# Optimization experiments

Hardware: AMD Instinct MI355X
Metric: run time of the kernel (lower is better)

The kernel has to match this reference:

```python
import jax, jax.numpy as jnp
import numpy as np

N_NODES = 50000
N_EDGES = 800000


def graph_conv(h, W, b, src, dst, n_nodes):
    # DGL GraphConv with norm='both':
    #   out = D_in^{-1/2} * A^T * (D_out^{-1/2} * h) @ W + b
    ones = jnp.ones((src.shape[0],), dtype=h.dtype)
    deg_out = jax.ops.segment_sum(ones, src, num_segments=n_nodes)
    deg_in = jax.ops.segment_sum(ones, dst, num_segments=n_nodes)
    norm_src = jnp.clip(deg_out, 1.0) ** -0.5  # [N]
    norm_dst = jnp.clip(deg_in, 1.0) ** -0.5   # [N]
    msg = (h * norm_src[:, None])[src]          # [E, F] gather
    agg = jax.ops.segment_sum(msg, dst, num_segments=n_nodes)  # [N, F] scatter
    return (agg * norm_dst[:, None]) @ W + b


def setup_inputs() -> dict:
    key = jax.random.key(0)
    ks = jax.random.split(key, 5)
    h = jax.random.normal(ks[0], (N_NODES, 64), dtype=jnp.float32)
    src = jax.random.randint(ks[1], (N_EDGES,), 0, N_NODES, dtype=jnp.int32)
    dst = jax.random.randint(ks[2], (N_EDGES,), 0, N_NODES, dtype=jnp.int32)
    W1 = jax.random.normal(ks[3], (64, 128), dtype=jnp.float32) * (1.0 / np.sqrt(64))
    b1 = jnp.zeros((128,), dtype=jnp.float32)
    W2 = jax.random.normal(ks[4], (128, 64), dtype=jnp.float32) * (1.0 / np.sqrt(128))
    b2 = jnp.zeros((64,), dtype=jnp.float32)
    return {"h": h, "src": src, "dst": dst, "W1": W1, "b1": b1, "W2": W2, "b2": b2}


def reference(h, src, dst, W1, b1, W2, b2):
    n = h.shape[0]
    h1 = jax.nn.relu(graph_conv(h, W1, b1, src, dst, n))
    out = graph_conv(h1, W2, b2, src, dst, n)
    return out
```

## Files before the change

### kernel.cpp

```cpp
#include <hip/hip_runtime.h>


#define NBMAX 512
#define CAPLOG 12
#define CAP (1 << CAPLOG)

typedef __attribute__((ext_vector_type(8))) short bf16x8;
typedef __attribute__((ext_vector_type(4))) float f32x4;

__device__ inline unsigned short f2bf(float f) {
    unsigned int u = __float_as_uint(f);
    unsigned int r = (u + 0x7FFFu + ((u >> 16) & 1u)) >> 16;
    return (unsigned short)r;
}
__device__ inline float bf2f_lo(unsigned int u) { return __uint_as_float(u << 16); }
__device__ inline float bf2f_hi(unsigned int u) { return __uint_as_float(u & 0xFFFF0000u); }
__device__ inline float bf2f(unsigned short h) {
    return __uint_as_float((unsigned int)h << 16);
}

__global__ __launch_bounds__(256) void place_direct(const int* __restrict__ src,
        const int* __restrict__ dst, int* __restrict__ cnt_s, int* __restrict__ cnt_d,
        unsigned char* __restrict__ ss, unsigned int* __restrict__ sd,
        int n_edges, int nb) {
    __shared__ int hs[NBMAX], hd[NBMAX], bs[NBMAX], bd[NBMAX];
    for (int i = threadIdx.x; i < nb; i += 256) { hs[i] = 0; hd[i] = 0; }
    __syncthreads();
    int chunk = (n_edges + gridDim.x - 1) / gridDim.x;
    int e0 = blockIdx.x * chunk;
    int e1 = e0 + chunk; if (e1 > n_edges) e1 = n_edges;
    for (int e = e0 + (int)threadIdx.x; e < e1; e += 256) {
        atomicAdd(&hs[src[e] >> 7], 1);
        atomicAdd(&hd[dst[e] >> 7], 1);
    }
    __syncthreads();
    for (int i = threadIdx.x; i < nb; i += 256) {
        int v = hs[i]; bs[i] = v ? atomicAdd(&cnt_s[i], v) : 0; hs[i] = 0;
        v = hd[i];     bd[i] = v ? atomicAdd(&cnt_d[i], v) : 0; hd[i] = 0;
    }
    __syncthreads();
    for (int e = e0 + (int)threadIdx.x; e < e1; e += 256) {
        int s = src[e], d = dst[e];
        int sb = s >> 7, db = d >> 7;
        int ps = bs[sb] + atomicAdd(&hs[sb], 1);
        ss[((size_t)sb << CAPLOG) + ps] = (unsigned char)(s & 127);
        int pd = bd[db] + atomicAdd(&hd[db], 1);
        sd[((size_t)db << CAPLOG) + pd] = ((unsigned int)(d & 127) << 25) | (unsigned int)s;
    }
}

__global__ __launch_bounds__(256) void prep(const float* __restrict__ h,
        const unsigned char* __restrict__ ss, const int* __restrict__ cnt_s,
        const unsigned int* __restrict__ sd, const int* __restrict__ cnt_d,
        float* __restrict__ norm_src, unsigned short* __restrict__ xb,
        int2* __restrict__ node_rng, unsigned short* __restrict__ srt,
        float* __restrict__ norm_dst, int n) {
    __shared__ int cnt[128], cur[128];
    __shared__ float nrm[128];
    __shared__ int w0tot;
    const int b = blockIdx.x;
    const int tid = threadIdx.x;

    if (tid < 128) cnt[tid] = 0;
    __syncthreads();
    {
        int used = cnt_s[b];
        const unsigned char* p = ss + ((size_t)b << CAPLOG);
        for (int i = tid; i < used; i += 256) atomicAdd(&cnt[p[i]], 1);
    }
    __syncthreads();
    if (tid < 128) {
        int c = cnt[tid]; if (c < 1) c = 1;
        float s = 1.0f / sqrtf((float)c);
        nrm[tid] = s;
        int node = (b << 7) + tid;
        if (node < n) norm_src[node] = s;
    }
    __syncthreads();
    {
        int base = b << 7;
        for (int t = tid; t < 128 * 16; t += 256) {
            int r = t >> 4, c4 = (t & 15) << 2;
            int node = base + r;
            if (node < n) {
                float s = nrm[r];
                float4 v = *(const float4*)(h + (size_t)node * 64 + c4);
                ushort4 o;
                o.x = f2bf(v.x * s); o.y = f2bf(v.y * s);
                o.z = f2bf(v.z * s); o.w = f2bf(v.w * s);
                *(ushort4*)(xb + (size_t)node * 64 + c4) = o;
            }
        }
    }
    __syncthreads();

    if (tid < 128) cnt[tid] = 0;
    __syncthreads();
    int used = cnt_d[b];
    const unsigned int* p = sd + ((size_t)b << CAPLOG);
    for (int i = tid; i < used; i += 256) atomicAdd(&cnt[p[i] >> 25], 1);
    __syncthreads();
    int lane = tid & 63, wid = tid >> 6;
    int v = (tid < 128) ? cnt[tid] : 0;
    int incl = v;
    #pragma unroll
    for (int d = 1; d < 64; d <<= 1) {
        int t = __shfl_up(incl, d, 64);
        if (lane >= d) incl += t;
    }
    if (tid == 63) w0tot = incl;
    __syncthreads();
    if (tid < 128) {
        int excl = incl - v + (wid == 1 ? w0tot : 0);
        cur[tid] = excl;
        int node = (b << 7) + tid;
        if (node < n) {
            int base = b << CAPLOG;
            node_rng[node] = make_int2(base + excl, base + excl + v);
            int c = v; if (c < 1) c = 1;
            norm_dst[node] = 1.0f / sqrtf((float)c);
        }
    }
    __syncthreads();
    for (int i = tid; i < used; i += 256) {
        unsigned int e = p[i];
        int l = (int)(e >> 25);
        int pos = atomicAdd(&cur[l], 1);
        srt[((size_t)b << CAPLOG) + pos] = (unsigned short)(e & 0xFFFFu);
    }
}

__global__ __launch_bounds__(256) void gather24(const unsigned short* __restrict__ xb,
        const unsigned short* __restrict__ srt, const int2* __restrict__ node_rng,
        const float* __restrict__ nrm, const float* __restrict__ bias,
        void* __restrict__ outp, int write_bf, int n_nodes) {
    int node = blockIdx.x * 4 + (threadIdx.x >> 6);
    if (node >= n_nodes) return;
    int lane = threadIdx.x & 63;
    int g  = lane >> 3;
    int c8 = (lane & 7) * 8;
    int2 rng = node_rng[node];
    int a0 = rng.x, a1 = rng.y;
    float acc[8];
    #pragma unroll
    for (int j = 0; j < 8; ++j) acc[j] = 0.f;
    for (int base = a0; base < a1; base += 24) {
        #pragma unroll
        for (int u = 0; u < 3; ++u) {
            int ei = base + u * 8 + g;
            int idx = ei < a1 ? ei : a1 - 1;
            float msk = ei < a1 ? 1.0f : 0.0f;
            int s = srt[idx];
            const uint4 v = *(const uint4*)(xb + (size_t)s * 64 + c8);
            acc[0] = fmaf(bf2f_lo(v.x), msk, acc[0]);
            acc[1] = fmaf(bf2f_hi(v.x), msk, acc[1]);
            acc[2] = fmaf(bf2f_lo(v.y), msk, acc[2]);
            acc[3] = fmaf(bf2f_hi(v.y), msk, acc[3]);
            acc[4] = fmaf(bf2f_lo(v.z), msk, acc[4]);
            acc[5] = fmaf(bf2f_hi(v.z), msk, acc[5]);
            acc[6] = fmaf(bf2f_lo(v.w), msk, acc[6]);
            acc[7] = fmaf(bf2f_hi(v.w), msk, acc[7]);
        }
    }
    #pragma unroll
    for (int off = 8; off < 64; off <<= 1) {
        #pragma unroll
        for (int j = 0; j < 8; ++j) acc[j] += __shfl_xor(acc[j], off, 64);
    }
    if (g == 0) {
        float s = nrm[node];
        float r[8];
        #pragma unroll
        for (int j = 0; j < 8; ++j) r[j] = acc[j] * s;
        if (write_bf) {
            unsigned short rb[8];
            #pragma unroll
            for (int j = 0; j < 8; ++j) rb[j] = f2bf(r[j]);
            unsigned short* o = (unsigned short*)outp + (size_t)node * 64 + c8;
            *(ushort4*)(o)     = make_ushort4(rb[0], rb[1], rb[2], rb[3]);
            *(ushort4*)(o + 4) = make_ushort4(rb[4], rb[5], rb[6], rb[7]);
        } else {
            if (bias) {
                #pragma unroll
                for (int j = 0; j < 8; ++j) r[j] += bias[c8 + j];
            }
            float* o = (float*)outp + (size_t)node * 64 + c8;
            *(float4*)(o)     = make_float4(r[0], r[1], r[2], r[3]);
            *(float4*)(o + 4) = make_float4(r[4], r[5], r[6], r[7]);
        }
    }
}

__global__ __launch_bounds__(256) void gemm12(const unsigned short* __restrict__ Ab,
        const float* __restrict__ W1, const float* __restrict__ b1,
        const float* __restrict__ norm, const float* __restrict__ W2,
        unsigned short* __restrict__ y2b, int n) {
    __shared__ unsigned short W1t[128 * 72];
    __shared__ unsigned short W2t[64 * 136];
    __shared__ unsigned short Hs[64 * 136];
    __shared__ float b1s[128];
    const int tid = threadIdx.x;

    for (int i = tid; i < 8192; i += 256) {
        int k = i >> 7, nn = i & 127;
        W1t[nn * 72 + k] = f2bf(W1[i]);
    }
    for (int i = tid; i < 8192; i += 256) {
        int k = i >> 6, nn = i & 63;
        W2t[nn * 136 + k] = f2bf(W2[i]);
    }
    if (tid < 128) b1s[tid] = b1[tid];
    __syncthreads();

    const int w  = tid >> 6;
    const int l  = tid & 63;
    const int ln = l & 15;
    const int q  = l >> 4;
    const int m0 = blockIdx.x * 64 + w * 16;

    int arow = m0 + ln; if (arow > n - 1) arow = n - 1;
    const unsigned short* arp = Ab + (size_t)arow * 64 + q * 8;
    bf16x8 a0 = *(const bf16x8*)(arp);
    bf16x8 a1 = *(const bf16x8*)(arp + 32);

    float ns[4];
    #pragma unroll
    for (int r = 0; r < 4; ++r) {
        int node = m0 + q * 4 + r;
        ns[r] = norm[node < n ? node : n - 1];
    }

    #pragma unroll
    for (int c = 0; c < 8; ++c) {
        const unsigned short* bp = W1t + (c * 16 + ln) * 72 + q * 8;
        bf16x8 b0 = *(const bf16x8*)(bp);
        bf16x8 bk = *(const bf16x8*)(bp + 32);
        f32x4 acc = {0.f, 0.f, 0.f, 0.f};
        acc = __builtin_amdgcn_mfma_f32_16x16x32_bf16(a0, b0, acc, 0, 0, 0);
        acc = __builtin_amdgcn_mfma_f32_16x16x32_bf16(a1, bk, acc, 0, 0, 0);
        int col = c * 16 + ln;
        float bb = b1s[col];
        #pragma unroll
        for (int r = 0; r < 4; ++r) {
            float v = acc[r] + bb;
            v = v > 0.f ? v : 0.f;
            Hs[(w * 16 + q * 4 + r) * 136 + col] = f2bf(v * ns[r]);
        }
    }
    __syncthreads();

    const unsigned short* hp = Hs + (size_t)(w * 16 + ln) * 136 + q * 8;
    bf16x8 h0 = *(const bf16x8*)(hp);
    bf16x8 h1 = *(const bf16x8*)(hp + 32);
    bf16x8 h2 = *(const bf16x8*)(hp + 64);
    bf16x8 h3 = *(const bf16x8*)(hp + 96);
    #pragma unroll
    for (int c = 0; c < 4; ++c) {
        const unsigned short* bp = W2t + (c * 16 + ln) * 136 + q * 8;
        f32x4 acc = {0.f, 0.f, 0.f, 0.f};
        acc = __builtin_amdgcn_mfma_f32_16x16x32_bf16(h0, *(const bf16x8*)(bp),      acc, 0, 0, 0);
        acc = __builtin_amdgcn_mfma_f32_16x16x32_bf16(h1, *(const bf16x8*)(bp + 32), acc, 0, 0, 0);
        acc = __builtin_amdgcn_mfma_f32_16x16x32_bf16(h2, *(const bf16x8*)(bp + 64), acc, 0, 0, 0);
        acc = __builtin_amdgcn_mfma_f32_16x16x32_bf16(h3, *(const bf16x8*)(bp + 96), acc, 0, 0, 0);
        #pragma unroll
        for (int r = 0; r < 4; ++r) {
            int node = m0 + q * 4 + r;
            if (node < n)
                y2b[(size_t)node * 64 + c * 16 + ln] = f2bf(acc[r]);
        }
    }
}

extern "C" void kernel_launch(void* const* d_in, const int* in_sizes, int n_in,
                              void* d_out, int out_size, void* d_ws, size_t ws_size,
                              hipStream_t stream) {
    const float* h   = (const float*)d_in[0];
    const int*   src = (const int*)d_in[1];
    const int*   dst = (const int*)d_in[2];
    const float* W1  = (const float*)d_in[3];
    const float* b1  = (const float*)d_in[4];
    const float* W2  = (const float*)d_in[5];
    const float* b2  = (const float*)d_in[6];
    float* out = (float*)d_out;

    const int n = in_sizes[0] / 64;
    const int E = in_sizes[1];
    const int nb = (n + 127) >> 7;

    char* p = (char*)d_ws;
    auto alloc = [&](size_t bytes) {
        void* r = (void*)p;
        p += (bytes + 255) & ~(size_t)255;
        return r;
    };
    float* norm_src      = (float*)alloc((size_t)n * 4);
    float* norm_dst      = (float*)alloc((size_t)n * 4);
    int2* node_rng       = (int2*)alloc((size_t)n * 8);
    int* cnt2            = (int*)alloc((size_t)2 * nb * 4);
    int* cnt_s = cnt2;
    int* cnt_d = cnt2 + nb;
    unsigned int* sd     = (unsigned int*)alloc((size_t)nb * CAP * 4);
    unsigned short* xb   = (unsigned short*)alloc((size_t)n * 64 * 2);
    unsigned short* agg1b= (unsigned short*)alloc((size_t)n * 64 * 2);
    unsigned short* y2b  = (unsigned short*)alloc((size_t)n * 64 * 2);
    unsigned short* srt  = (unsigned short*)alloc((size_t)nb * CAP * 2);
    unsigned char* ssb   = (unsigned char*)alloc((size_t)nb * CAP);

    hipMemsetAsync(cnt2, 0, 2 * (size_t)nb * sizeof(int), stream);

    place_direct<<<256, 256, 0, stream>>>(src, dst, cnt_s, cnt_d, ssb, sd, E, nb);
    prep<<<nb, 256, 0, stream>>>(h, ssb, cnt_s, sd, cnt_d, norm_src, xb,
                                 node_rng, srt, norm_dst, n);

    int gb = (n + 3) / 4;
    gather24<<<gb, 256, 0, stream>>>(xb, srt, node_rng, norm_dst, nullptr,
                                     (void*)agg1b, 1, n);

    int tb = (n + 63) / 64;
    gemm12<<<tb, 256, 0, stream>>>(agg1b, W1, b1, norm_src, W2, y2b, n);

    gather24<<<gb, 256, 0, stream>>>(y2b, srt, node_rng, norm_dst, b2,
                                     (void*)out, 0, n);
}
```

Baseline: 168.6 us.

## Split node features into two 32-column planes and gather each plane separately

Feature tables (xb, y2b) are stored as two separate 32-wide bf16 planes, and each sparse gather now runs twice, once per plane. Each pass touches a 3.2 MB table instead of 6.4 MB, so the random-access working set is more likely to stay in cache. Each wave now covers 16 edges per step instead of 8. In exchange, the edge index list and node ranges are read twice and there are two more kernel launches.

Result: slower. 206.8 us (+22.7%).

```diff
diff --git a/kernel.cpp b/kernel.cpp
--- a/kernel.cpp
+++ b/kernel.cpp
@@ -15,9 +15,6 @@
 }
 __device__ inline float bf2f_lo(unsigned int u) { return __uint_as_float(u << 16); }
 __device__ inline float bf2f_hi(unsigned int u) { return __uint_as_float(u & 0xFFFF0000u); }
-__device__ inline float bf2f(unsigned short h) {
-    return __uint_as_float((unsigned int)h << 16);
-}
 
 __global__ __launch_bounds__(256) void place_direct(const int* __restrict__ src,
         const int* __restrict__ dst, int* __restrict__ cnt_s, int* __restrict__ cnt_d,
@@ -52,7 +49,8 @@
 __global__ __launch_bounds__(256) void prep(const float* __restrict__ h,
         const unsigned char* __restrict__ ss, const int* __restrict__ cnt_s,
         const unsigned int* __restrict__ sd, const int* __restrict__ cnt_d,
-        float* __restrict__ norm_src, unsigned short* __restrict__ xb,
+        float* __restrict__ norm_src, unsigned short* __restrict__ xlo,
+        unsigned short* __restrict__ xhi,
         int2* __restrict__ node_rng, unsigned short* __restrict__ srt,
         float* __restrict__ norm_dst, int n) {
     __shared__ int cnt[128], cur[128];
@@ -80,15 +78,18 @@
     {
         int base = b << 7;
         for (int t = tid; t < 128 * 16; t += 256) {
-            int r = t >> 4, c4 = (t & 15) << 2;
+            int r = t >> 4, q = t & 15;
             int node = base + r;
             if (node < n) {
                 float s = nrm[r];
-                float4 v = *(const float4*)(h + (size_t)node * 64 + c4);
+                float4 v = *(const float4*)(h + (size_t)node * 64 + q * 4);
                 ushort4 o;
                 o.x = f2bf(v.x * s); o.y = f2bf(v.y * s);
                 o.z = f2bf(v.z * s); o.w = f2bf(v.w * s);
-                *(ushort4*)(xb + (size_t)node * 64 + c4) = o;
+                unsigned short* dst = (q < 8)
+                    ? xlo + (size_t)node * 32 + q * 4
+                    : xhi + (size_t)node * 32 + (q - 8) * 4;
+                *(ushort4*)dst = o;
             }
         }
     }
@@ -130,28 +131,29 @@
     }
 }
 
-__global__ __launch_bounds__(256) void gather24(const unsigned short* __restrict__ xb,
+__global__ __launch_bounds__(256) void gather_plane(
+        const unsigned short* __restrict__ xp,
         const unsigned short* __restrict__ srt, const int2* __restrict__ node_rng,
         const float* __restrict__ nrm, const float* __restrict__ bias,
-        void* __restrict__ outp, int write_bf, int n_nodes) {
+        void* __restrict__ outp, int out_off, int write_bf, int n_nodes) {
     int node = blockIdx.x * 4 + (threadIdx.x >> 6);
     if (node >= n_nodes) return;
     int lane = threadIdx.x & 63;
-    int g  = lane >> 3;
-    int c8 = (lane & 7) * 8;
+    int g  = lane >> 2;
+    int c8 = (lane & 3) * 8;
     int2 rng = node_rng[node];
     int a0 = rng.x, a1 = rng.y;
     float acc[8];
     #pragma unroll
     for (int j = 0; j < 8; ++j) acc[j] = 0.f;
-    for (int base = a0; base < a1; base += 24) {
-        #pragma unroll
-        for (int u = 0; u < 3; ++u) {
-            int ei = base + u * 8 + g;
+    for (int base = a0; base < a1; base += 32) {
+        #pragma unroll
+        for (int u = 0; u < 2; ++u) {
+            int ei = base + u * 16 + g;
             int idx = ei < a1 ? ei : a1 - 1;
             float msk = ei < a1 ? 1.0f : 0.0f;
             int s = srt[idx];
-            const uint4 v = *(const uint4*)(xb + (size_t)s * 64 + c8);
+            const uint4 v = *(const uint4*)(xp + (size_t)s * 32 + c8);
             acc[0] = fmaf(bf2f_lo(v.x), msk, acc[0]);
             acc[1] = fmaf(bf2f_hi(v.x), msk, acc[1]);
             acc[2] = fmaf(bf2f_lo(v.y), msk, acc[2]);
@@ -163,7 +165,7 @@
         }
     }
     #pragma unroll
-    for (int off = 8; off < 64; off <<= 1) {
+    for (int off = 4; off < 64; off <<= 1) {
         #pragma unroll
         for (int j = 0; j < 8; ++j) acc[j] += __shfl_xor(acc[j], off, 64);
     }
@@ -176,15 +178,13 @@
             unsigned short rb[8];
             #pragma unroll
             for (int j = 0; j < 8; ++j) rb[j] = f2bf(r[j]);
-            unsigned short* o = (unsigned short*)outp + (size_t)node * 64 + c8;
+            unsigned short* o = (unsigned short*)outp + (size_t)node * 64 + out_off + c8;
             *(ushort4*)(o)     = make_ushort4(rb[0], rb[1], rb[2], rb[3]);
             *(ushort4*)(o + 4) = make_ushort4(rb[4], rb[5], rb[6], rb[7]);
         } else {
-            if (bias) {
-                #pragma unroll
-                for (int j = 0; j < 8; ++j) r[j] += bias[c8 + j];
-            }
-            float* o = (float*)outp + (size_t)node * 64 + c8;
+            #pragma unroll
+            for (int j = 0; j < 8; ++j) r[j] += bias[c8 + j];
+            float* o = (float*)outp + (size_t)node * 64 + out_off + c8;
             *(float4*)(o)     = make_float4(r[0], r[1], r[2], r[3]);
             *(float4*)(o + 4) = make_float4(r[4], r[5], r[6], r[7]);
         }
@@ -194,7 +194,7 @@
 __global__ __launch_bounds__(256) void gemm12(const unsigned short* __restrict__ Ab,
         const float* __restrict__ W1, const float* __restrict__ b1,
         const float* __restrict__ norm, const float* __restrict__ W2,
-        unsigned short* __restrict__ y2b, int n) {
+        unsigned short* __restrict__ y2lo, unsigned short* __restrict__ y2hi, int n) {
     __shared__ unsigned short W1t[128 * 72];
     __shared__ unsigned short W2t[64 * 136];
     __shared__ unsigned short Hs[64 * 136];
@@ -262,11 +262,13 @@
         acc = __builtin_amdgcn_mfma_f32_16x16x32_bf16(h1, *(const bf16x8*)(bp + 32), acc, 0, 0, 0);
         acc = __builtin_amdgcn_mfma_f32_16x16x32_bf16(h2, *(const bf16x8*)(bp + 64), acc, 0, 0, 0);
         acc = __builtin_amdgcn_mfma_f32_16x16x32_bf16(h3, *(const bf16x8*)(bp + 96), acc, 0, 0, 0);
+        unsigned short* plane = (c < 2) ? y2lo : y2hi;
+        int pcol = (c & 1) * 16 + ln;
         #pragma unroll
         for (int r = 0; r < 4; ++r) {
             int node = m0 + q * 4 + r;
             if (node < n)
-                y2b[(size_t)node * 64 + c * 16 + ln] = f2bf(acc[r]);
+                plane[(size_t)node * 32 + pcol] = f2bf(acc[r]);
         }
     }
 }
@@ -300,25 +302,31 @@
     int* cnt_s = cnt2;
     int* cnt_d = cnt2 + nb;
     unsigned int* sd     = (unsigned int*)alloc((size_t)nb * CAP * 4);
-    unsigned short* xb   = (unsigned short*)alloc((size_t)n * 64 * 2);
+    unsigned short* xlo  = (unsigned short*)alloc((size_t)n * 32 * 2);
+    unsigned short* xhi  = (unsigned short*)alloc((size_t)n * 32 * 2);
     unsigned short* agg1b= (unsigned short*)alloc((size_t)n * 64 * 2);
-    unsigned short* y2b  = (unsigned short*)alloc((size_t)n * 64 * 2);
+    unsigned short* y2lo = (unsigned short*)alloc((size_t)n * 32 * 2);
+    unsigned short* y2hi = (unsigned short*)alloc((size_t)n * 32 * 2);
     unsigned short* srt  = (unsigned short*)alloc((size_t)nb * CAP * 2);
     unsigned char* ssb   = (unsigned char*)alloc((size_t)nb * CAP);
 
     hipMemsetAsync(cnt2, 0, 2 * (size_t)nb * sizeof(int), stream);
 
     place_direct<<<256, 256, 0, stream>>>(src, dst, cnt_s, cnt_d, ssb, sd, E, nb);
-    prep<<<nb, 256, 0, stream>>>(h, ssb, cnt_s, sd, cnt_d, norm_src, xb,
+    prep<<<nb, 256, 0, stream>>>(h, ssb, cnt_s, sd, cnt_d, norm_src, xlo, xhi,
                                  node_rng, srt, norm_dst, n);
 
     int gb = (n + 3) / 4;
-    gather24<<<gb, 256, 0, stream>>>(xb, srt, node_rng, norm_dst, nullptr,
-                                     (void*)agg1b, 1, n);
+    gather_plane<<<gb, 256, 0, stream>>>(xlo, srt, node_rng, norm_dst, nullptr,
+                                         (void*)agg1b, 0, 1, n);
+    gather_plane<<<gb, 256, 0, stream>>>(xhi, srt, node_rng, norm_dst, nullptr,
+                                         (void*)agg1b, 32, 1, n);
 
     int tb = (n + 63) / 64;
-    gemm12<<<tb, 256, 0, stream>>>(agg1b, W1, b1, norm_src, W2, y2b, n);
-
-    gather24<<<gb, 256, 0, stream>>>(y2b, srt, node_rng, norm_dst, b2,
-                                     (void*)out, 0, n);
-}
+    gemm12<<<tb, 256, 0, stream>>>(agg1b, W1, b1, norm_src, W2, y2lo, y2hi, n);
+
+    gather_plane<<<gb, 256, 0, stream>>>(y2lo, srt, node_rng, norm_dst, b2,
+                                         (void*)out, 0, 0, n);
+    gather_plane<<<gb, 256, 0, stream>>>(y2hi, srt, node_rng, norm_dst, b2 + 32,
+                                         (void*)out, 32, 0, n);
+}
```

## Fuse first-layer gather into GEMM kernel and precompute bf16 transposed weights

Applied to the files above, without the earlier changes.

Merges the first aggregation gather with the two-layer MFMA GEMM: each block gathers 64 destination rows into shared memory and immediately multiplies them, removing the intermediate bf16 aggregate buffer and one launch. Weight conversion and transposition to bf16 moves into the prep kernel so GEMM blocks read pre-converted weights from global memory instead of rebuilding them in LDS per block. The risk is reduced parallelism in the latency-bound gather, since each wave now processes 16 nodes sequentially with far fewer blocks.

Result: slower. 178.1 us (+5.6%).

```diff
diff --git a/kernel.cpp b/kernel.cpp
--- a/kernel.cpp
+++ b/kernel.cpp
@@ -15,9 +15,6 @@
 }
 __device__ inline float bf2f_lo(unsigned int u) { return __uint_as_float(u << 16); }
 __device__ inline float bf2f_hi(unsigned int u) { return __uint_as_float(u & 0xFFFF0000u); }
-__device__ inline float bf2f(unsigned short h) {
-    return __uint_as_float((unsigned int)h << 16);
-}
 
 __global__ __launch_bounds__(256) void place_direct(const int* __restrict__ src,
         const int* __restrict__ dst, int* __restrict__ cnt_s, int* __restrict__ cnt_d,
@@ -54,12 +51,26 @@
         const unsigned int* __restrict__ sd, const int* __restrict__ cnt_d,
         float* __restrict__ norm_src, unsigned short* __restrict__ xb,
         int2* __restrict__ node_rng, unsigned short* __restrict__ srt,
-        float* __restrict__ norm_dst, int n) {
+        float* __restrict__ norm_dst,
+        const float* __restrict__ W1, const float* __restrict__ W2,
+        unsigned short* __restrict__ w1t, unsigned short* __restrict__ w2t, int n) {
     __shared__ int cnt[128], cur[128];
     __shared__ float nrm[128];
     __shared__ int w0tot;
     const int b = blockIdx.x;
     const int tid = threadIdx.x;
+
+    {
+        int idx = b * 256 + tid;
+        if (idx < 8192) {
+            int k = idx >> 7, nn = idx & 127;
+            w1t[nn * 64 + k] = f2bf(W1[idx]);
+        } else if (idx < 16384) {
+            int j = idx - 8192;
+            int k = j >> 6, nn = j & 63;
+            w2t[nn * 128 + k] = f2bf(W2[j]);
+        }
+    }
 
     if (tid < 128) cnt[tid] = 0;
     __syncthreads();
@@ -130,10 +141,131 @@
     }
 }
 
+__global__ __launch_bounds__(256) void gather_gemm(
+        const unsigned short* __restrict__ xb,
+        const unsigned short* __restrict__ srt, const int2* __restrict__ node_rng,
+        const float* __restrict__ norm_dst, const float* __restrict__ norm_src,
+        const unsigned short* __restrict__ w1t, const float* __restrict__ b1,
+        const unsigned short* __restrict__ w2t,
+        unsigned short* __restrict__ y2b, int n) {
+    __shared__ unsigned short As[64 * 72];
+    __shared__ unsigned short Hs[64 * 136];
+    __shared__ float b1s[128];
+    const int tid = threadIdx.x;
+    if (tid < 128) b1s[tid] = b1[tid];
+
+    const int w = tid >> 6;
+    const int l = tid & 63;
+    const int m0 = blockIdx.x * 64;
+
+    {
+        int g  = l >> 3;
+        int c8 = (l & 7) * 8;
+        for (int i = 0; i < 16; ++i) {
+            int row = w * 16 + i;
+            int node = m0 + row;
+            int nd = node < n ? node : n - 1;
+            int2 rng = node_rng[nd];
+            int a0 = rng.x, a1 = rng.y;
+            float acc[8];
+            #pragma unroll
+            for (int j = 0; j < 8; ++j) acc[j] = 0.f;
+            for (int base = a0; base < a1; base += 24) {
+                #pragma unroll
+                for (int u = 0; u < 3; ++u) {
+                    int ei = base + u * 8 + g;
+                    int idx = ei < a1 ? ei : a1 - 1;
+                    float msk = ei < a1 ? 1.0f : 0.0f;
+                    int s = srt[idx];
+                    const uint4 v = *(const uint4*)(xb + (size_t)s * 64 + c8);
+                    acc[0] = fmaf(bf2f_lo(v.x), msk, acc[0]);
+                    acc[1] = fmaf(bf2f_hi(v.x), msk, acc[1]);
+                    acc[2] = fmaf(bf2f_lo(v.y), msk, acc[2]);
+                    acc[3] = fmaf(bf2f_hi(v.y), msk, acc[3]);
+                    acc[4] = fmaf(bf2f_lo(v.z), msk, acc[4]);
+                    acc[5] = fmaf(bf2f_hi(v.z), msk, acc[5]);
+                    acc[6] = fmaf(bf2f_lo(v.w), msk, acc[6]);
+                    acc[7] = fmaf(bf2f_hi(v.w), msk, acc[7]);
+                }
+            }
+            #pragma unroll
+            for (int off = 8; off < 64; off <<= 1) {
+                #pragma unroll
+                for (int j = 0; j < 8; ++j) acc[j] += __shfl_xor(acc[j], off, 64);
+            }
+            if (g == 0) {
+                float s = norm_dst[nd];
+                unsigned short rb[8];
+                #pragma unroll
+                for (int j = 0; j < 8; ++j) rb[j] = f2bf(acc[j] * s);
+                unsigned short* o = As + row * 72 + c8;
+                *(ushort4*)(o)     = make_ushort4(rb[0], rb[1], rb[2], rb[3]);
+                *(ushort4*)(o + 4) = make_ushort4(rb[4], rb[5], rb[6], rb[7]);
+            }
+        }
+    }
+    __syncthreads();
+
+    const int ln = l & 15;
+    const int q  = l >> 4;
+    const int mb = m0 + w * 16;
+
+    const unsigned short* arp = As + (w * 16 + ln) * 72 + q * 8;
+    bf16x8 a0 = *(const bf16x8*)(arp);
+    bf16x8 a1 = *(const bf16x8*)(arp + 32);
+
+    float ns[4];
+    #pragma unroll
+    for (int r = 0; r < 4; ++r) {
+        int node = mb + q * 4 + r;
+        ns[r] = norm_src[node < n ? node : n - 1];
+    }
+
+    #pragma unroll
+    for (int c = 0; c < 8; ++c) {
+        const unsigned short* bp = w1t + (size_t)(c * 16 + ln) * 64 + q * 8;
+        bf16x8 b0 = *(const bf16x8*)(bp);
+        bf16x8 bk = *(const bf16x8*)(bp + 32);
+        f32x4 acc = {0.f, 0.f, 0.f, 0.f};
+        acc = __builtin_amdgcn_mfma_f32_16x16x32_bf16(a0, b0, acc, 0, 0, 0);
+        acc = __builtin_amdgcn_mfma_f32_16x16x32_bf16(a1, bk, acc, 0, 0, 0);
+        int col = c * 16 + ln;
+        float bb = b1s[col];
+        #pragma unroll
+        for (int r = 0; r < 4; ++r) {
+            float v = acc[r] + bb;
+            v = v > 0.f ? v : 0.f;
+            Hs[(w * 16 + q * 4 + r) * 136 + col] = f2bf(v * ns[r]);
+        }
+    }
+    __syncthreads();
+
+    const unsigned short* hp = Hs + (size_t)(w * 16 + ln) * 136 + q * 8;
+    bf16x8 h0 = *(const bf16x8*)(hp);
+    bf16x8 h1 = *(const bf16x8*)(hp + 32);
+    bf16x8 h2 = *(const bf16x8*)(hp + 64);
+    bf16x8 h3 = *(const bf16x8*)(hp + 96);
+    #pragma unroll
+    for (int c = 0; c < 4; ++c) {
+        const unsigned short* bp = w2t + (size_t)(c * 16 + ln) * 128 + q * 8;
+        f32x4 acc = {0.f, 0.f, 0.f, 0.f};
+        acc = __builtin_amdgcn_mfma_f32_16x16x32_bf16(h0, *(const bf16x8*)(bp),      acc, 0, 0, 0);
+        acc = __builtin_amdgcn_mfma_f32_16x16x32_bf16(h1, *(const bf16x8*)(bp + 32), acc, 0, 0, 0);
+        acc = __builtin_amdgcn_mfma_f32_16x16x32_bf16(h2, *(const bf16x8*)(bp + 64), acc, 0, 0, 0);
+        acc = __builtin_amdgcn_mfma_f32_16x16x32_bf16(h3, *(const bf16x8*)(bp + 96), acc, 0, 0, 0);
+        #pragma unroll
+        for (int r = 0; r < 4; ++r) {
+            int node = mb + q * 4 + r;
+            if (node < n)
+                y2b[(size_t)node * 64 + c * 16 + ln] = f2bf(acc[r]);
+        }
+    }
+}
+
 __global__ __launch_bounds__(256) void gather24(const unsigned short* __restrict__ xb,
         const unsigned short* __restrict__ srt, const int2* __restrict__ node_rng,
         const float* __restrict__ nrm, const float* __restrict__ bias,
-        void* __restrict__ outp, int write_bf, int n_nodes) {
+        float* __restrict__ outp, int n_nodes) {
     int node = blockIdx.x * 4 + (threadIdx.x >> 6);
     if (node >= n_nodes) return;
     int lane = threadIdx.x & 63;
@@ -171,103 +303,10 @@
         float s = nrm[node];
         float r[8];
         #pragma unroll
-        for (int j = 0; j < 8; ++j) r[j] = acc[j] * s;
-        if (write_bf) {
-            unsigned short rb[8];
-            #pragma unroll
-            for (int j = 0; j < 8; ++j) rb[j] = f2bf(r[j]);
-            unsigned short* o = (unsigned short*)outp + (size_t)node * 64 + c8;
-            *(ushort4*)(o)     = make_ushort4(rb[0], rb[1], rb[2], rb[3]);
-            *(ushort4*)(o + 4) = make_ushort4(rb[4], rb[5], rb[6], rb[7]);
-        } else {
-            if (bias) {
-                #pragma unroll
-                for (int j = 0; j < 8; ++j) r[j] += bias[c8 + j];
-            }
-            float* o = (float*)outp + (size_t)node * 64 + c8;
-            *(float4*)(o)     = make_float4(r[0], r[1], r[2], r[3]);
-            *(float4*)(o + 4) = make_float4(r[4], r[5], r[6], r[7]);
-        }
-    }
-}
-
-__global__ __launch_bounds__(256) void gemm12(const unsigned short* __restrict__ Ab,
-        const float* __restrict__ W1, const float* __restrict__ b1,
-        const float* __restrict__ norm, const float* __restrict__ W2,
-        unsigned short* __restrict__ y2b, int n) {
-    __shared__ unsigned short W1t[128 * 72];
-    __shared__ unsigned short W2t[64 * 136];
-    __shared__ unsigned short Hs[64 * 136];
-    __shared__ float b1s[128];
-    const int tid = threadIdx.x;
-
-    for (int i = tid; i < 8192; i += 256) {
-        int k = i >> 7, nn = i & 127;
-        W1t[nn * 72 + k] = f2bf(W1[i]);
-    }
-    for (int i = tid; i < 8192; i += 256) {
-        int k = i >> 6, nn = i & 63;
-        W2t[nn * 136 + k] = f2bf(W2[i]);
-    }
-    if (tid < 128) b1s[tid] = b1[tid];
-    __syncthreads();
-
-    const int w  = tid >> 6;
-    const int l  = tid & 63;
-    const int ln = l & 15;
-    const int q  = l >> 4;
-    const int m0 = blockIdx.x * 64 + w * 16;
-
-    int arow = m0 + ln; if (arow > n - 1) arow = n - 1;
-    const unsigned short* arp = Ab + (size_t)arow * 64 + q * 8;
-    bf16x8 a0 = *(const bf16x8*)(arp);
-    bf16x8 a1 = *(const bf16x8*)(arp + 32);
-
-    float ns[4];
-    #pragma unroll
-    for (int r = 0; r < 4; ++r) {
-        int node = m0 + q * 4 + r;
-        ns[r] = norm[node < n ? node : n - 1];
-    }
-
-    #pragma unroll
-    for (int c = 0; c < 8; ++c) {
-        const unsigned short* bp = W1t + (c * 16 + ln) * 72 + q * 8;
-        bf16x8 b0 = *(const bf16x8*)(bp);
-        bf16x8 bk = *(const bf16x8*)(bp + 32);
-        f32x4 acc = {0.f, 0.f, 0.f, 0.f};
-        acc = __builtin_amdgcn_mfma_f32_16x16x32_bf16(a0, b0, acc, 0, 0, 0);
-        acc = __builtin_amdgcn_mfma_f32_16x16x32_bf16(a1, bk, acc, 0, 0, 0);
-        int col = c * 16 + ln;
-        float bb = b1s[col];
-        #pragma unroll
-        for (int r = 0; r < 4; ++r) {
-            float v = acc[r] + bb;
-            v = v > 0.f ? v : 0.f;
-            Hs[(w * 16 + q * 4 + r) * 136 + col] = f2bf(v * ns[r]);
-        }
-    }
-    __syncthreads();
-
-    const unsigned short* hp = Hs + (size_t)(w * 16 + ln) * 136 + q * 8;
-    bf16x8 h0 = *(const bf16x8*)(hp);
-    bf16x8 h1 = *(const bf16x8*)(hp + 32);
-    bf16x8 h2 = *(const bf16x8*)(hp + 64);
-    bf16x8 h3 = *(const bf16x8*)(hp + 96);
-    #pragma unroll
-    for (int c = 0; c < 4; ++c) {
-        const unsigned short* bp = W2t + (c * 16 + ln) * 136 + q * 8;
-        f32x4 acc = {0.f, 0.f, 0.f, 0.f};
-        acc = __builtin_amdgcn_mfma_f32_16x16x32_bf16(h0, *(const bf16x8*)(bp),      acc, 0, 0, 0);
-        acc = __builtin_amdgcn_mfma_f32_16x16x32_bf16(h1, *(const bf16x8*)(bp + 32), acc, 0, 0, 0);
-        acc = __builtin_amdgcn_mfma_f32_16x16x32_bf16(h2, *(const bf16x8*)(bp + 64), acc, 0, 0, 0);
-        acc = __builtin_amdgcn_mfma_f32_16x16x32_bf16(h3, *(const bf16x8*)(bp + 96), acc, 0, 0, 0);
-        #pragma unroll
-        for (int r = 0; r < 4; ++r) {
-            int node = m0 + q * 4 + r;
-            if (node < n)
-                y2b[(size_t)node * 64 + c * 16 + ln] = f2bf(acc[r]);
-        }
+        for (int j = 0; j < 8; ++j) r[j] = acc[j] * s + bias[c8 + j];
+        float* o = outp + (size_t)node * 64 + c8;
+        *(float4*)(o)     = make_float4(r[0], r[1], r[2], r[3]);
+        *(float4*)(o + 4) = make_float4(r[4], r[5], r[6], r[7]);
     }
 }
 
@@ -301,24 +340,22 @@
     int* cnt_d = cnt2 + nb;
     unsigned int* sd     = (unsigned int*)alloc((size_t)nb * CAP * 4);
     unsigned short* xb   = (unsigned short*)alloc((size_t)n * 64 * 2);
-    unsigned short* agg1b= (unsigned short*)alloc((size_t)n * 64 * 2);
     unsigned short* y2b  = (unsigned short*)alloc((size_t)n * 64 * 2);
     unsigned short* srt  = (unsigned short*)alloc((size_t)nb * CAP * 2);
     unsigned char* ssb   = (unsigned char*)alloc((size_t)nb * CAP);
+    unsigned short* w1t  = (unsigned short*)alloc(8192 * 2);
+    unsigned short* w2t  = (unsigned short*)alloc(8192 * 2);
 
     hipMemsetAsync(cnt2, 0, 2 * (size_t)nb * sizeof(int), stream);
 
     place_direct<<<256, 256, 0, stream>>>(src, dst, cnt_s, cnt_d, ssb, sd, E, nb);
     prep<<<nb, 256, 0, stream>>>(h, ssb, cnt_s, sd, cnt_d, norm_src, xb,
-                                 node_rng, srt, norm_dst, n);
+                                 node_rng, srt, norm_dst, W1, W2, w1t, w2t, n);
+
+    int tb = (n + 63) / 64;
+    gather_gemm<<<tb, 256, 0, stream>>>(xb, srt, node_rng, norm_dst, norm_src,
+                                        w1t, b1, w2t, y2b, n);
 
     int gb = (n + 3) / 4;
-    gather24<<<gb, 256, 0, stream>>>(xb, srt, node_rng, norm_dst, nullptr,
-                                     (void*)agg1b, 1, n);
-
-    int tb = (n + 63) / 64;
-    gemm12<<<tb, 256, 0, stream>>>(agg1b, W1, b1, norm_src, W2, y2b, n);
-
-    gather24<<<gb, 256, 0, stream>>>(y2b, srt, node_rng, norm_dst, b2,
-                                     (void*)out, 0, n);
-}
+    gather24<<<gb, 256, 0, stream>>>(y2b, srt, node_rng, norm_dst, b2, out, n);
+}
```
